# Kernel tuning notes

Measured on AMD Instinct MI355X. Metric: run time of the kernel, lower is better.

## Reference

```python
import jax, jax.numpy as jnp
import numpy as np

N = 50000      # num nodes
E = 800000     # num edges (avg degree 16)
IN, H, OUT = 128, 128, 16
R = 8          # num relations


def rgcn_conv(x, edge_index, edge_type, W, root, bias, num_relations):
    """PyG RGCNConv with aggr='mean': out = x@root + bias + sum_r mean_{j in N_r(i)} x_j @ W_r.
    Mean is linear, so aggregate raw x_j per relation first, then one matmul per relation."""
    src, dst = edge_index[0], edge_index[1]  # messages flow src -> dst
    x_src = x[src]                            # [E, F] gather
    out = x @ root + bias                     # root/self term
    for r in range(num_relations):            # small fixed loop over relations
        m = (edge_type == r).astype(x.dtype)  # [E]
        s = jax.ops.segment_sum(x_src * m[:, None], dst, num_segments=x.shape[0])  # [N, F]
        c = jax.ops.segment_sum(m, dst, num_segments=x.shape[0])                   # [N]
        out = out + (s / jnp.maximum(c, 1.0)[:, None]) @ W[r]
    return out


def setup_inputs() -> dict:
    key = jax.random.key(0)
    ks = jax.random.split(key, 12)
    glorot = lambda k, shape: jax.random.normal(k, shape, jnp.float32) * (2.0 / (shape[-2] + shape[-1])) ** 0.5
    return {
        "x": jax.random.normal(ks[0], (N, IN), jnp.float32),
        "edge_index": jax.random.randint(ks[1], (2, E), 0, N, jnp.int64) if jax.config.read('jax_enable_x64') else jax.random.randint(ks[1], (2, E), 0, N).astype(jnp.int32),
        "edge_type": jax.random.randint(ks[2], (E,), 0, R).astype(jnp.int32),
        "w0": glorot(ks[3], (R, IN, H)),
        "root0": glorot(ks[4], (IN, H)),
        "b0": jnp.zeros((H,), jnp.float32),
        "w1": glorot(ks[5], (R, H, H)),
        "root1": glorot(ks[6], (H, H)),
        "b1": jnp.zeros((H,), jnp.float32),
        "w2": glorot(ks[7], (R, H, OUT)),
        "root2": glorot(ks[8], (H, OUT)),
        "b2": jnp.zeros((OUT,), jnp.float32),
    }


def reference(x, edge_index, edge_type, w0, root0, b0, w1, root1, b1, w2, root2, b2):
    # layer 0: in -> hidden, relu (dropout is identity in eval mode)
    h = jax.nn.relu(rgcn_conv(x, edge_index, edge_type, w0, root0, b0, R))
    # layer 1: hidden -> hidden, relu
    h = jax.nn.relu(rgcn_conv(h, edge_index, edge_type, w1, root1, b1, R))
    # layer 2: hidden -> out (no activation)
    return rgcn_conv(h, edge_index, edge_type, w2, root2, b2, R)
```

## Files before the change

### kernel.cpp

```cpp
#include <hip/hip_runtime.h>

#define N_NODES 50000
#define N_EDGES 800000
#define NREL 8
#define NB8 (N_NODES * NREL)
#define SCAN_T 12500
#define KSTEPS 36
#define A_STRIDE 1160
#define NTILES (N_NODES / 16)

typedef __attribute__((ext_vector_type(8))) short short8;
typedef __attribute__((ext_vector_type(4))) float f32x4;
typedef __attribute__((ext_vector_type(2))) float f32x2;

__device__ __forceinline__ unsigned short f2bf(float v) {
    union { float f; unsigned int u; } c; c.f = v;
    return (unsigned short)((c.u + 0x7FFFu + ((c.u >> 16) & 1u)) >> 16);
}
__device__ __forceinline__ float bfhi2f(unsigned int u) {
    union { unsigned int u; float f; } c; c.u = u & 0xFFFF0000u; return c.f;
}
__device__ __forceinline__ float bflo2f(unsigned int u) {
    union { unsigned int u; float f; } c; c.u = u << 16; return c.f;
}

#define PREP_Z   (NB8 / 4)
#define PREP_X   (N_NODES * 32)
#define PREP_P   (8 * KSTEPS * 64)
#define PREP_P2  (1 * KSTEPS * 64)
#define PREP_TOTAL (PREP_Z + PREP_X + 2 * PREP_P + PREP_P2)

__device__ __forceinline__ void pack_one(int idx, const float* __restrict__ root,
                                         const float* __restrict__ W,
                                         unsigned short* __restrict__ Wpack, int FOUT) {
    int lane = idx & 63;
    int ks = (idx >> 6) % KSTEPS;
    int ct = idx / (KSTEPS * 64);
    int kbase = ks * 32 + (lane >> 4) * 8;
    int col = ct * 16 + (lane & 15);
    union { unsigned short us[8]; uint4 v; } u;
#pragma unroll
    for (int j = 0; j < 8; j++) {
        int k = kbase + j;
        float val = (k < 128) ? root[(size_t)k * FOUT + col]
                              : W[(size_t)(k - 128) * FOUT + col];
        u.us[j] = f2bf(val);
    }
    ((uint4*)Wpack)[idx] = u.v;
}

__global__ void prep_kernel(const float* __restrict__ X, unsigned int* __restrict__ Xb2,
                            const float* __restrict__ r0, const float* __restrict__ w0,
                            unsigned short* __restrict__ Wp0,
                            const float* __restrict__ r1, const float* __restrict__ w1,
                            unsigned short* __restrict__ Wp1,
                            const float* __restrict__ r2, const float* __restrict__ w2,
                            unsigned short* __restrict__ Wp2,
                            int* __restrict__ cnt) {
    int t = blockIdx.x * blockDim.x + threadIdx.x;
    if (t < PREP_Z) { ((int4*)cnt)[t] = make_int4(0, 0, 0, 0); return; }
    t -= PREP_Z;
    if (t < PREP_X) {
        float4 v = ((const float4*)X)[t];
        unsigned int p0 = (unsigned int)f2bf(v.x) | ((unsigned int)f2bf(v.y) << 16);
        unsigned int p1 = (unsigned int)f2bf(v.z) | ((unsigned int)f2bf(v.w) << 16);
        ((uint2*)Xb2)[t] = make_uint2(p0, p1);
        return;
    }
    t -= PREP_X;
    if (t < PREP_P) { pack_one(t, r0, w0, Wp0, 128); return; }
    t -= PREP_P;
    if (t < PREP_P) { pack_one(t, r1, w1, Wp1, 128); return; }
    t -= PREP_P;
    if (t < PREP_P2) pack_one(t, r2, w2, Wp2, 16);
}

__global__ void rank_kernel(const int* __restrict__ ei, const int* __restrict__ et,
                            int* __restrict__ cnt, int* __restrict__ rank, int E) {
    int e = blockIdx.x * blockDim.x + threadIdx.x;
    if (e >= E) return;
    int d = ei[E + e];
    int t = et[e];
    rank[e] = atomicAdd(&cnt[d * NREL + t], 1);
}

__global__ void scanA_kernel(const int* __restrict__ cnt, int* __restrict__ tsum) {
    int g = blockIdx.x * blockDim.x + threadIdx.x;
    if (g >= SCAN_T) return;
    const int4* p = (const int4*)(cnt + (size_t)g * 32);
    int s = 0;
#pragma unroll
    for (int j = 0; j < 8; j++) {
        int4 v = p[j];
        s += v.x + v.y + v.z + v.w;
    }
    tsum[g] = s;
}

__global__ void scanB_kernel(const int* __restrict__ tsum, int* __restrict__ toff) {
    __shared__ int part[1024];
    int t = threadIdx.x;
    const int C = 13;
    int n0 = t * C, n1 = n0 + C; if (n1 > SCAN_T) n1 = SCAN_T;
    int s = 0;
    for (int n = n0; n < n1; n++) s += tsum[n];
    part[t] = s;
    __syncthreads();
    for (int off = 1; off < 1024; off <<= 1) {
        int v = (t >= off) ? part[t - off] : 0;
        __syncthreads();
        part[t] += v;
        __syncthreads();
    }
    int run = (t > 0) ? part[t - 1] : 0;
    for (int n = n0; n < n1; n++) { toff[n] = run; run += tsum[n]; }
}

__global__ void scanC_kernel(const int* __restrict__ cnt, const int* __restrict__ toff,
                             int* __restrict__ rs8) {
    int g = blockIdx.x * blockDim.x + threadIdx.x;
    if (g >= SCAN_T) return;
    int run = toff[g];
    int base = g * 32;
#pragma unroll 4
    for (int j = 0; j < 32; j++) {
        rs8[base + j] = run;
        run += cnt[base + j];
    }
    if (g == 0) rs8[NB8] = N_EDGES;
}

__global__ void place_kernel(const int* __restrict__ ei, const int* __restrict__ et,
                             const int* __restrict__ rank, const int* __restrict__ rs8,
                             unsigned short* __restrict__ csr_src, int E) {
    int e = blockIdx.x * blockDim.x + threadIdx.x;
    if (e >= E) return;
    int s = ei[e];
    int d = ei[E + e];
    int t = et[e];
    csr_src[rs8[d * NREL + t] + rank[e]] = (unsigned short)s;
}

template <int FOUT, bool RELU>
__global__ __launch_bounds__(512, 8) void layer_kernel(
    const unsigned int* __restrict__ Xb2,
    const int* __restrict__ rs8,
    const unsigned short* __restrict__ csr_src,
    const unsigned short* __restrict__ Wpack,
    const float* __restrict__ bias,
    void* __restrict__ Yout)
{
    __shared__ __align__(16) unsigned short Abuf[16][A_STRIDE];

    int tid = threadIdx.x;
    int wave = tid >> 6, lane = tid & 63;
    int l15 = lane & 15;
    int node0 = blockIdx.x * 16;

    {
        int gn0 = node0 + wave * 2;
        unsigned int* row0 = (unsigned int*)&Abuf[wave * 2][0];
        unsigned int* row1 = (unsigned int*)&Abuf[wave * 2 + 1][0];

        int bl = lane <= 16 ? lane : 16;
        int bv = rs8[gn0 * 8 + bl];
        unsigned int self0 = Xb2[(size_t)gn0 * 64 + lane];
        unsigned int self1 = Xb2[(size_t)(gn0 + 1) * 64 + lane];

        int e     = __builtin_amdgcn_readlane(bv, 0);
        int e_end = __builtin_amdgcn_readlane(bv, 16);

        row0[lane] = self0;
        row1[lane] = self1;

        int r = 0;
        int segs = e;
        int be = __builtin_amdgcn_readlane(bv, 1);
        f32x2 av = (f32x2){0.f, 0.f};

#define FLUSH_R()                                                              \
        do {                                                                   \
            int c_ = be - segs;                                                \
            float iv_ = 1.0f / (float)(c_ > 0 ? c_ : 1);                       \
            unsigned int pk_ = (unsigned int)f2bf(av.x * iv_)                  \
                             | ((unsigned int)f2bf(av.y * iv_) << 16);         \
            unsigned int* rw_ = (r < 8) ? row0 : row1;                         \
            rw_[(1 + (r & 7)) * 64 + lane] = pk_;                              \
            av = (f32x2){0.f, 0.f}; segs = be; r++;                            \
            be = __builtin_amdgcn_readlane(bv, r + 1 <= 16 ? r + 1 : 16);      \
        } while (0)

        if (e < e_end) {
            int e1m = e_end - 1;
            int ma = e + l15; if (ma > e1m) ma = e1m;
            unsigned int mv = csr_src[ma];
            while (e < e_end) {
                int bn = e_end - e; if (bn > 16) bn = 16;
                int sc[16];
#pragma unroll
                for (int k = 0; k < 16; k++) sc[k] = __builtin_amdgcn_readlane((int)mv, k);
                unsigned int xp[16];
#pragma unroll
                for (int k = 0; k < 16; k++) xp[k] = Xb2[(size_t)sc[k] * 64 + lane];
                int en = e + bn;
                if (en < e_end) {
                    int mb = en + l15; if (mb > e1m) mb = e1m;
                    mv = csr_src[mb];
                }
#pragma unroll
                for (int k = 0; k < 16; k++) {
                    if (k < bn) {
                        int ec = e + k;
                        while (ec >= be) FLUSH_R();
                        av += (f32x2){bflo2f(xp[k]), bfhi2f(xp[k])};
                    }
                }
                e = en;
            }
        }
        while (r < 16) FLUSH_R();
#undef FLUSH_R
    }
    __syncthreads();

    int quad = lane >> 4, l16 = lane & 15;
    if constexpr (FOUT == 128) {
        int ct = wave;
        f32x4 acc = (f32x4){0.f, 0.f, 0.f, 0.f};
        for (int ks = 0; ks < KSTEPS; ks++) {
            short8 b = *(const short8*)(Wpack + (((size_t)ct * KSTEPS + ks) * 64 + lane) * 8);
            short8 a = *(const short8*)&Abuf[l16][ks * 32 + quad * 8];
            acc = __builtin_amdgcn_mfma_f32_16x16x32_bf16(a, b, acc, 0, 0, 0);
        }
        unsigned short* Yb = (unsigned short*)Yout;
        int h = ct * 16 + l16;
        float bvs = bias[h];
#pragma unroll
        for (int r4 = 0; r4 < 4; r4++) {
            int node = node0 + quad * 4 + r4;
            float v = acc[r4] + bvs;
            if (RELU) v = v > 0.f ? v : 0.f;
            Yb[(size_t)node * 128 + h] = f2bf(v);
        }
    } else {
        int ks0 = wave * 4 + (wave < 4 ? wave : 4);
        int ksn = (wave < 4) ? 5 : 4;
        f32x4 acc = (f32x4){0.f, 0.f, 0.f, 0.f};
        for (int ks = ks0; ks < ks0 + ksn; ks++) {
            short8 b = *(const short8*)(Wpack + ((size_t)ks * 64 + lane) * 8);
            short8 a = *(const short8*)&Abuf[l16][ks * 32 + quad * 8];
            acc = __builtin_amdgcn_mfma_f32_16x16x32_bf16(a, b, acc, 0, 0, 0);
        }
        __syncthreads();
        float* red = (float*)&Abuf[0][0];
#pragma unroll
        for (int r4 = 0; r4 < 4; r4++) red[(wave * 64 + lane) * 4 + r4] = acc[r4];
        __syncthreads();
        if (tid < 256) {
            int reg = tid >> 6, l = tid & 63;
            float s = 0.f;
#pragma unroll
            for (int w = 0; w < 8; w++) s += red[(w * 64 + l) * 4 + reg];
            int node = node0 + ((l >> 4) << 2) + reg;
            int h = l & 15;
            float v = s + bias[h];
            if (RELU) v = v > 0.f ? v : 0.f;
            ((float*)Yout)[(size_t)node * 16 + h] = v;
        }
    }
}

extern "C" void kernel_launch(void* const* d_in, const int* in_sizes, int n_in,
                              void* d_out, int out_size, void* d_ws, size_t ws_size,
                              hipStream_t stream) {
    const float* x  = (const float*)d_in[0];
    const int*   ei = (const int*)d_in[1];
    const int*   et = (const int*)d_in[2];
    const float* w0 = (const float*)d_in[3];
    const float* r0 = (const float*)d_in[4];
    const float* b0 = (const float*)d_in[5];
    const float* w1 = (const float*)d_in[6];
    const float* r1 = (const float*)d_in[7];
    const float* b1 = (const float*)d_in[8];
    const float* w2 = (const float*)d_in[9];
    const float* r2 = (const float*)d_in[10];
    const float* b2 = (const float*)d_in[11];

    char* wsp = (char*)d_ws;
    size_t off = 0;
    auto alloc = [&](size_t bytes) -> void* {
        void* p = wsp + off;
        off += (bytes + 255) & ~(size_t)255;
        return p;
    };

    int* cnt    = (int*)alloc((size_t)NB8 * 4);
    int* rs8    = (int*)alloc(((size_t)NB8 + 1) * 4);
    int* rank   = (int*)alloc((size_t)N_EDGES * 4);
    int* tsum   = (int*)alloc((size_t)SCAN_T * 4);
    int* toff   = (int*)alloc((size_t)SCAN_T * 4);
    unsigned short* csr_src = (unsigned short*)alloc((size_t)N_EDGES * 2);
    unsigned short* Wp0 = (unsigned short*)alloc((size_t)8 * KSTEPS * 64 * 8 * 2);
    unsigned short* Wp1 = (unsigned short*)alloc((size_t)8 * KSTEPS * 64 * 8 * 2);
    unsigned short* Wp2 = (unsigned short*)alloc((size_t)1 * KSTEPS * 64 * 8 * 2);
    unsigned int* Xb = (unsigned int*)alloc((size_t)N_NODES * 64 * 4);
    unsigned int* H0 = (unsigned int*)alloc((size_t)N_NODES * 64 * 4);
    unsigned int* H1 = (unsigned int*)alloc((size_t)N_NODES * 64 * 4);

    prep_kernel<<<dim3((PREP_TOTAL + 255) / 256), dim3(256), 0, stream>>>(
        x, Xb, r0, w0, Wp0, r1, w1, Wp1, r2, w2, Wp2, cnt);
    rank_kernel<<<dim3((N_EDGES + 255) / 256), dim3(256), 0, stream>>>(ei, et, cnt, rank, N_EDGES);
    scanA_kernel<<<dim3((SCAN_T + 255) / 256), dim3(256), 0, stream>>>(cnt, tsum);
    scanB_kernel<<<dim3(1), dim3(1024), 0, stream>>>(tsum, toff);
    scanC_kernel<<<dim3((SCAN_T + 255) / 256), dim3(256), 0, stream>>>(cnt, toff, rs8);
    place_kernel<<<dim3((N_EDGES + 255) / 256), dim3(256), 0, stream>>>(ei, et, rank, rs8,
                                                                        csr_src, N_EDGES);

    layer_kernel<128, true ><<<dim3(NTILES), dim3(512), 0, stream>>>(
        Xb, rs8, csr_src, Wp0, b0, (void*)H0);
    layer_kernel<128, true ><<<dim3(NTILES), dim3(512), 0, stream>>>(
        H0, rs8, csr_src, Wp1, b1, (void*)H1);
    layer_kernel<16, false><<<dim3(NTILES), dim3(512), 0, stream>>>(
        H1, rs8, csr_src, Wp2, b2, d_out);
}
```

Baseline: 322.4 us.

## Fuse CSR build into one persistent kernel and precompute inverse counts

Five CSR-construction kernels (rank, three scan phases, place) are merged into a single persistent kernel of 512 blocks that uses atomic-flag grid barriers between phases. This removes per-launch gaps and tail effects. The scan phase also precomputes per-(node,relation) reciprocal counts, so the layer kernels read them instead of dividing. The layer kernels additionally fetch 64 edge sources per load instead of 16, replace the round-to-nearest-even bf16 pack with a cheaper round-half-up perm, and use shift/or indexing. The spin-wait grid barrier relies on all 512 blocks being co-resident, and the new rounding changes numerics slightly.

```diff
diff --git a/kernel.cpp b/kernel.cpp
--- a/kernel.cpp
+++ b/kernel.cpp
@@ -8,6 +8,7 @@
 #define KSTEPS 36
 #define A_STRIDE 1160
 #define NTILES (N_NODES / 16)
+#define BGRID 512
 
 typedef __attribute__((ext_vector_type(8))) short short8;
 typedef __attribute__((ext_vector_type(4))) float f32x4;
@@ -22,6 +23,12 @@
 }
 __device__ __forceinline__ float bflo2f(unsigned int u) {
     union { unsigned int u; float f; } c; c.u = u << 16; return c.f;
+}
+__device__ __forceinline__ unsigned fbits(float v) {
+    union { float f; unsigned u; } c; c.f = v; return c.u;
+}
+__device__ __forceinline__ float bitsf(int u) {
+    union { int i; float f; } c; c.i = u; return c.f;
 }
 
 #define PREP_Z   (NB8 / 4)
@@ -56,8 +63,9 @@
                             unsigned short* __restrict__ Wp1,
                             const float* __restrict__ r2, const float* __restrict__ w2,
                             unsigned short* __restrict__ Wp2,
-                            int* __restrict__ cnt) {
+                            int* __restrict__ cnt, int* __restrict__ flags) {
     int t = blockIdx.x * blockDim.x + threadIdx.x;
+    if (blockIdx.x == 0 && threadIdx.x < 8) flags[threadIdx.x] = 0;
     if (t < PREP_Z) { ((int4*)cnt)[t] = make_int4(0, 0, 0, 0); return; }
     t -= PREP_Z;
     if (t < PREP_X) {
@@ -75,76 +83,97 @@
     if (t < PREP_P2) pack_one(t, r2, w2, Wp2, 16);
 }
 
-__global__ void rank_kernel(const int* __restrict__ ei, const int* __restrict__ et,
-                            int* __restrict__ cnt, int* __restrict__ rank, int E) {
-    int e = blockIdx.x * blockDim.x + threadIdx.x;
-    if (e >= E) return;
-    int d = ei[E + e];
-    int t = et[e];
-    rank[e] = atomicAdd(&cnt[d * NREL + t], 1);
-}
-
-__global__ void scanA_kernel(const int* __restrict__ cnt, int* __restrict__ tsum) {
-    int g = blockIdx.x * blockDim.x + threadIdx.x;
-    if (g >= SCAN_T) return;
-    const int4* p = (const int4*)(cnt + (size_t)g * 32);
-    int s = 0;
-#pragma unroll
-    for (int j = 0; j < 8; j++) {
-        int4 v = p[j];
-        s += v.x + v.y + v.z + v.w;
-    }
-    tsum[g] = s;
-}
-
-__global__ void scanB_kernel(const int* __restrict__ tsum, int* __restrict__ toff) {
-    __shared__ int part[1024];
-    int t = threadIdx.x;
-    const int C = 13;
-    int n0 = t * C, n1 = n0 + C; if (n1 > SCAN_T) n1 = SCAN_T;
-    int s = 0;
-    for (int n = n0; n < n1; n++) s += tsum[n];
-    part[t] = s;
+__device__ __forceinline__ void gbar(int* flag, int n, int tid) {
     __syncthreads();
-    for (int off = 1; off < 1024; off <<= 1) {
-        int v = (t >= off) ? part[t - off] : 0;
+    if (tid == 0) {
+        __threadfence();
+        atomicAdd(flag, 1);
+        while (atomicAdd(flag, 0) < n) {}
+        __threadfence();
+    }
+    __syncthreads();
+}
+
+__global__ __launch_bounds__(256) void build_kernel(
+    const int* __restrict__ ei, const int* __restrict__ et,
+    int* __restrict__ cnt, int* __restrict__ rank,
+    int* __restrict__ tsum, int* __restrict__ toff,
+    int* __restrict__ rs8, float* __restrict__ inv8,
+    unsigned short* __restrict__ csr_src, int* __restrict__ flags)
+{
+    int tid = threadIdx.x;
+    int gid = blockIdx.x * 256 + tid;
+    const int T = BGRID * 256;
+
+    for (int e = gid; e < N_EDGES; e += T) {
+        int d = ei[N_EDGES + e];
+        int ty = et[e];
+        rank[e] = atomicAdd(&cnt[d * NREL + ty], 1);
+    }
+    gbar(&flags[0], BGRID, tid);
+
+    for (int g = gid; g < SCAN_T; g += T) {
+        const int4* p = (const int4*)(cnt + (size_t)g * 32);
+        int s = 0;
+#pragma unroll
+        for (int j = 0; j < 8; j++) {
+            int4 v = p[j];
+            s += v.x + v.y + v.z + v.w;
+        }
+        tsum[g] = s;
+    }
+    gbar(&flags[1], BGRID, tid);
+
+    if (blockIdx.x == 0) {
+        __shared__ int part[256];
+        const int C = (SCAN_T + 255) / 256;
+        int n0 = tid * C, n1 = n0 + C; if (n1 > SCAN_T) n1 = SCAN_T;
+        int s = 0;
+        for (int n = n0; n < n1; n++) s += tsum[n];
+        part[tid] = s;
         __syncthreads();
-        part[t] += v;
+        for (int off = 1; off < 256; off <<= 1) {
+            int v = (tid >= off) ? part[tid - off] : 0;
+            __syncthreads();
+            part[tid] += v;
+            __syncthreads();
+        }
+        int run = (tid > 0) ? part[tid - 1] : 0;
+        for (int n = n0; n < n1; n++) { toff[n] = run; run += tsum[n]; }
+        __threadfence();
         __syncthreads();
-    }
-    int run = (t > 0) ? part[t - 1] : 0;
-    for (int n = n0; n < n1; n++) { toff[n] = run; run += tsum[n]; }
-}
-
-__global__ void scanC_kernel(const int* __restrict__ cnt, const int* __restrict__ toff,
-                             int* __restrict__ rs8) {
-    int g = blockIdx.x * blockDim.x + threadIdx.x;
-    if (g >= SCAN_T) return;
-    int run = toff[g];
-    int base = g * 32;
+        if (tid == 0) atomicAdd(&flags[2], 1);
+    }
+    if (tid == 0) { while (atomicAdd(&flags[2], 0) < 1) {} __threadfence(); }
+    __syncthreads();
+
+    for (int g = gid; g < SCAN_T; g += T) {
+        int run = toff[g];
+        int base = g * 32;
 #pragma unroll 4
-    for (int j = 0; j < 32; j++) {
-        rs8[base + j] = run;
-        run += cnt[base + j];
-    }
-    if (g == 0) rs8[NB8] = N_EDGES;
-}
-
-__global__ void place_kernel(const int* __restrict__ ei, const int* __restrict__ et,
-                             const int* __restrict__ rank, const int* __restrict__ rs8,
-                             unsigned short* __restrict__ csr_src, int E) {
-    int e = blockIdx.x * blockDim.x + threadIdx.x;
-    if (e >= E) return;
-    int s = ei[e];
-    int d = ei[E + e];
-    int t = et[e];
-    csr_src[rs8[d * NREL + t] + rank[e]] = (unsigned short)s;
+        for (int j = 0; j < 32; j++) {
+            int c = cnt[base + j];
+            rs8[base + j] = run;
+            inv8[base + j] = 1.0f / (float)(c > 0 ? c : 1);
+            run += c;
+        }
+    }
+    if (gid == 0) rs8[NB8] = N_EDGES;
+    gbar(&flags[3], BGRID, tid);
+
+    for (int e = gid; e < N_EDGES; e += T) {
+        int s = ei[e];
+        int d = ei[N_EDGES + e];
+        int ty = et[e];
+        csr_src[rs8[d * NREL + ty] + rank[e]] = (unsigned short)s;
+    }
 }
 
 template <int FOUT, bool RELU>
 __global__ __launch_bounds__(512, 8) void layer_kernel(
     const unsigned int* __restrict__ Xb2,
     const int* __restrict__ rs8,
+    const float* __restrict__ inv8,
     const unsigned short* __restrict__ csr_src,
     const unsigned short* __restrict__ Wpack,
     const float* __restrict__ bias,
@@ -164,8 +193,9 @@
 
         int bl = lane <= 16 ? lane : 16;
         int bv = rs8[gn0 * 8 + bl];
-        unsigned int self0 = Xb2[(size_t)gn0 * 64 + lane];
-        unsigned int self1 = Xb2[(size_t)(gn0 + 1) * 64 + lane];
+        int invi = ((const int*)inv8)[gn0 * 8 + l15];
+        unsigned int self0 = Xb2[((unsigned)gn0 << 6) | lane];
+        unsigned int self1 = Xb2[((unsigned)(gn0 + 1) << 6) | lane];
 
         int e     = __builtin_amdgcn_readlane(bv, 0);
         int e_end = __builtin_amdgcn_readlane(bv, 16);
@@ -174,38 +204,42 @@
         row1[lane] = self1;
 
         int r = 0;
-        int segs = e;
         int be = __builtin_amdgcn_readlane(bv, 1);
         f32x2 av = (f32x2){0.f, 0.f};
 
 #define FLUSH_R()                                                              \
         do {                                                                   \
-            int c_ = be - segs;                                                \
-            float iv_ = 1.0f / (float)(c_ > 0 ? c_ : 1);                       \
-            unsigned int pk_ = (unsigned int)f2bf(av.x * iv_)                  \
-                             | ((unsigned int)f2bf(av.y * iv_) << 16);         \
+            float iv_ = bitsf(__builtin_amdgcn_readlane(invi, r));             \
+            unsigned ux_ = fbits(av.x * iv_) + 0x8000u;                        \
+            unsigned uy_ = fbits(av.y * iv_) + 0x8000u;                        \
+            unsigned pk_ = __builtin_amdgcn_perm(uy_, ux_, 0x07060302u);       \
             unsigned int* rw_ = (r < 8) ? row0 : row1;                         \
             rw_[(1 + (r & 7)) * 64 + lane] = pk_;                              \
-            av = (f32x2){0.f, 0.f}; segs = be; r++;                            \
+            av = (f32x2){0.f, 0.f}; r++;                                       \
             be = __builtin_amdgcn_readlane(bv, r + 1 <= 16 ? r + 1 : 16);      \
         } while (0)
 
         if (e < e_end) {
             int e1m = e_end - 1;
-            int ma = e + l15; if (ma > e1m) ma = e1m;
+            int ma = e + lane; if (ma > e1m) ma = e1m;
             unsigned int mv = csr_src[ma];
+            int wbase = e;
             while (e < e_end) {
                 int bn = e_end - e; if (bn > 16) bn = 16;
+                int koff = e - wbase;
                 int sc[16];
 #pragma unroll
-                for (int k = 0; k < 16; k++) sc[k] = __builtin_amdgcn_readlane((int)mv, k);
+                for (int k = 0; k < 16; k++)
+                    sc[k] = __builtin_amdgcn_readlane((int)mv, koff + k);
                 unsigned int xp[16];
 #pragma unroll
-                for (int k = 0; k < 16; k++) xp[k] = Xb2[(size_t)sc[k] * 64 + lane];
+                for (int k = 0; k < 16; k++)
+                    xp[k] = Xb2[((unsigned)sc[k] << 6) | lane];
                 int en = e + bn;
-                if (en < e_end) {
-                    int mb = en + l15; if (mb > e1m) mb = e1m;
+                if (koff + bn == 64 && en < e_end) {
+                    int mb = en + lane; if (mb > e1m) mb = e1m;
                     mv = csr_src[mb];
+                    wbase = en;
                 }
 #pragma unroll
                 for (int k = 0; k < 16; k++) {
@@ -296,9 +330,11 @@
 
     int* cnt    = (int*)alloc((size_t)NB8 * 4);
     int* rs8    = (int*)alloc(((size_t)NB8 + 1) * 4);
+    float* inv8 = (float*)alloc((size_t)NB8 * 4);
     int* rank   = (int*)alloc((size_t)N_EDGES * 4);
     int* tsum   = (int*)alloc((size_t)SCAN_T * 4);
     int* toff   = (int*)alloc((size_t)SCAN_T * 4);
+    int* flags  = (int*)alloc(8 * 4);
     unsigned short* csr_src = (unsigned short*)alloc((size_t)N_EDGES * 2);
     unsigned short* Wp0 = (unsigned short*)alloc((size_t)8 * KSTEPS * 64 * 8 * 2);
     unsigned short* Wp1 = (unsigned short*)alloc((size_t)8 * KSTEPS * 64 * 8 * 2);
@@ -308,18 +344,14 @@
     unsigned int* H1 = (unsigned int*)alloc((size_t)N_NODES * 64 * 4);
 
     prep_kernel<<<dim3((PREP_TOTAL + 255) / 256), dim3(256), 0, stream>>>(
-        x, Xb, r0, w0, Wp0, r1, w1, Wp1, r2, w2, Wp2, cnt);
-    rank_kernel<<<dim3((N_EDGES + 255) / 256), dim3(256), 0, stream>>>(ei, et, cnt, rank, N_EDGES);
-    scanA_kernel<<<dim3((SCAN_T + 255) / 256), dim3(256), 0, stream>>>(cnt, tsum);
-    scanB_kernel<<<dim3(1), dim3(1024), 0, stream>>>(tsum, toff);
-    scanC_kernel<<<dim3((SCAN_T + 255) / 256), dim3(256), 0, stream>>>(cnt, toff, rs8);
-    place_kernel<<<dim3((N_EDGES + 255) / 256), dim3(256), 0, stream>>>(ei, et, rank, rs8,
-                                                                        csr_src, N_EDGES);
+        x, Xb, r0, w0, Wp0, r1, w1, Wp1, r2, w2, Wp2, cnt, flags);
+    build_kernel<<<dim3(BGRID), dim3(256), 0, stream>>>(
+        ei, et, cnt, rank, tsum, toff, rs8, inv8, csr_src, flags);
 
     layer_kernel<128, true ><<<dim3(NTILES), dim3(512), 0, stream>>>(
-        Xb, rs8, csr_src, Wp0, b0, (void*)H0);
+        Xb, rs8, inv8, csr_src, Wp0, b0, (void*)H0);
     layer_kernel<128, true ><<<dim3(NTILES), dim3(512), 0, stream>>>(
-        H0, rs8, csr_src, Wp1, b1, (void*)H1);
+        H0, rs8, inv8, csr_src, Wp1, b1, (void*)H1);
     layer_kernel<16, false><<<dim3(NTILES), dim3(512), 0, stream>>>(
-        H1, rs8, csr_src, Wp2, b2, d_out);
-}
+        H1, rs8, inv8, csr_src, Wp2, b2, d_out);
+}
```

Measured after the change: 463.2 us. +43.7%, slower.
